# Kernel tuning notes

Measured on AMD Instinct MI355X. Metric: run time of the kernel, lower is better.

## Reference

```python
import jax, jax.numpy as jnp
import numpy as np

HID = 128
OUT = 5


def _gru_layer(x, kernel, rkernel, bias):
    # Keras GRU v2 semantics, reset_after=True, activation=tanh, recurrent_activation=sigmoid.
    # x: [B, T, F]; kernel: [F, 3H]; rkernel: [H, 3H]; bias: [2, 3H] (input bias, recurrent bias)
    b_in, b_rec = bias[0], bias[1]
    H = rkernel.shape[0]
    xw = jnp.einsum('btf,fh->bth', x, kernel) + b_in  # precompute input projections [B,T,3H]

    def step(h, xw_t):
        ri = h @ rkernel + b_rec                      # [B, 3H]
        xz, xr, xh = jnp.split(xw_t, 3, axis=-1)
        rz, rr, rh = jnp.split(ri, 3, axis=-1)
        z = jax.nn.sigmoid(xz + rz)
        r = jax.nn.sigmoid(xr + rr)
        hh = jnp.tanh(xh + r * rh)
        h_new = z * h + (1.0 - z) * hh
        return h_new, h_new

    h0 = jnp.zeros((x.shape[0], H), dtype=x.dtype)
    _, hs = jax.lax.scan(step, h0, jnp.swapaxes(xw, 0, 1))  # [T, B, H]
    return jnp.swapaxes(hs, 0, 1)                           # [B, T, H]


def setup_inputs() -> dict:
    key = jax.random.key(0)
    ks = jax.random.split(key, 12)
    B, T, F = 64, 2048, 128
    s = 1.0 / np.sqrt(F)
    inp = {"x": jax.random.normal(ks[0], (B, T, F), dtype=jnp.float32)}
    for i in range(3):
        fin = F if i == 0 else HID
        inp[f"k{i}"] = jax.random.normal(ks[1 + 3 * i], (fin, 3 * HID), dtype=jnp.float32) * s
        inp[f"rk{i}"] = jax.random.normal(ks[2 + 3 * i], (HID, 3 * HID), dtype=jnp.float32) * s
        inp[f"b{i}"] = jnp.zeros((2, 3 * HID), dtype=jnp.float32)
    inp["wo"] = jax.random.normal(ks[10], (HID, OUT), dtype=jnp.float32) * s
    inp["bo"] = jnp.zeros((OUT,), dtype=jnp.float32)
    return inp


def reference(x, k0, rk0, b0, k1, rk1, b1, k2, rk2, b2, wo, bo):
    h = _gru_layer(x, k0, rk0, b0)
    h = _gru_layer(h, k1, rk1, b1)
    h = _gru_layer(h, k2, rk2, b2)
    return h @ wo + bo  # [B, T, OUT]
```

## Files before the change

### kernel.cpp

```cpp
#include <hip/hip_runtime.h>
#include <hip/hip_bf16.h>
#include <hip/hip_fp16.h>


#define HID   128
#define H3    384
#define OUTD  5
#define CHK   16

typedef _Float16 f16x2 __attribute__((ext_vector_type(2)));
typedef _Float16 f16x8 __attribute__((ext_vector_type(8)));

__device__ __forceinline__ float fdot2(f16x2 a, f16x2 b, float c) {
#if __has_builtin(__builtin_amdgcn_fdot2)
    return __builtin_amdgcn_fdot2(a, b, c, false);
#else
    return fmaf((float)a.x, (float)b.x, fmaf((float)a.y, (float)b.y, c));
#endif
}

__device__ __forceinline__ float fexp2(float x) {
#if __has_builtin(__builtin_amdgcn_exp2f)
    return __builtin_amdgcn_exp2f(x);
#else
    return exp2f(x);
#endif
}

__device__ __forceinline__ float frcp(float x) {
#if __has_builtin(__builtin_amdgcn_rcpf)
    return __builtin_amdgcn_rcpf(x);
#else
    return 1.f / x;
#endif
}

__device__ __forceinline__ float fsigmoid(float x) {
    return frcp(1.f + fexp2(x * -1.4426950408889634f));
}

__device__ __forceinline__ float ftanh_(float x) {
    return fmaf(-2.f, frcp(1.f + fexp2(x * 2.8853900817779268f)), 1.f);
}

__device__ __forceinline__ void soft_barrier() {
    asm volatile("s_waitcnt lgkmcnt(0)\n\ts_barrier" ::: "memory");
}

__device__ __forceinline__ float quad_sum(float x) {
#if __has_builtin(__builtin_amdgcn_mov_dpp)
    int i1 = __builtin_amdgcn_mov_dpp(__float_as_int(x), 0xB1, 0xF, 0xF, true);
    x += __int_as_float(i1);
    int i2 = __builtin_amdgcn_mov_dpp(__float_as_int(x), 0x4E, 0xF, 0xF, true);
    x += __int_as_float(i2);
#else
    x += __shfl_xor(x, 1);
    x += __shfl_xor(x, 2);
#endif
    return x;
}

__global__ void zero_flags(int* f) {
    if (threadIdx.x < 192) f[threadIdx.x] = 0;
}

__global__ __launch_bounds__(512, 2) void gru_pipe(
    const float* __restrict__ x,
    const float* __restrict__ k0, const float* __restrict__ k1, const float* __restrict__ k2,
    const float* __restrict__ rk0, const float* __restrict__ rk1, const float* __restrict__ rk2,
    const float* __restrict__ b0, const float* __restrict__ b1, const float* __restrict__ b2,
    _Float16* __restrict__ hpl0, _Float16* __restrict__ hpl1, _Float16* __restrict__ hpl2,
    int* flags, int T)
{
    const int blk   = blockIdx.x;
    const int layer = blk >> 6;
    const int b     = blk & 63;
    const int t     = threadIdx.x;
    const int j     = t >> 2;
    const int kh    = t & 3;
    const int k0i   = kh * 32;
    const int NC    = T / CHK;

    const float* Kw = (layer == 0) ? k0  : (layer == 1) ? k1  : k2;
    const float* Rw = (layer == 0) ? rk0 : (layer == 1) ? rk1 : rk2;
    const float* Bs = (layer == 0) ? b0  : (layer == 1) ? b1  : b2;
    const _Float16* hin = (layer == 1) ? hpl0 : hpl1;
    _Float16* hout = (layer == 0) ? hpl0 : (layer == 1) ? hpl1 : hpl2;

    __shared__ __align__(16) _Float16 hb[2][HID];
    __shared__ __align__(16) _Float16 ins[2][CHK][HID];

    f16x2 wzR[16], wrR[16], whR[16], wzK[16], wrK[16], whK[16];
#pragma unroll
    for (int p = 0; p < 16; ++p) {
        const int k = k0i + 2 * p;
        const float* r0p = Rw + (size_t)k * H3;
        const float* r1p = Rw + (size_t)(k + 1) * H3;
        const float* k0p = Kw + (size_t)k * H3;
        const float* k1p = Kw + (size_t)(k + 1) * H3;
        f16x2 a;
        a.x = (_Float16)r0p[j];       a.y = (_Float16)r1p[j];       wzR[p] = a;
        a.x = (_Float16)r0p[j + 128]; a.y = (_Float16)r1p[j + 128]; wrR[p] = a;
        a.x = (_Float16)r0p[j + 256]; a.y = (_Float16)r1p[j + 256]; whR[p] = a;
        a.x = (_Float16)k0p[j];       a.y = (_Float16)k1p[j];       wzK[p] = a;
        a.x = (_Float16)k0p[j + 128]; a.y = (_Float16)k1p[j + 128]; wrK[p] = a;
        a.x = (_Float16)k0p[j + 256]; a.y = (_Float16)k1p[j + 256]; whK[p] = a;
    }
    const float bzK = Bs[j]       + Bs[384 + j];
    const float brK = Bs[128 + j] + Bs[384 + 128 + j];
    const float bhK = Bs[256 + j];
    const float bhR = Bs[384 + 256 + j];

    int* myflag = flags + layer * 64 + b;
    int* sflag  = flags + (layer - 1) * 64 + b;

    const float*    xb  = x    + (size_t)b * T * HID;
    const _Float16* hib = hin  + (size_t)b * T * HID;
    _Float16*       hob = hout + (size_t)b * T * HID;

    f16x2 sreg[2];
    auto stage_load = [&](int cc) {
#pragma unroll
        for (int i = 0; i < 2; ++i) {
            const int d  = t + 512 * i;
            const int rw = d >> 6;
            const int c2 = d & 63;
            const size_t off = (size_t)(cc * CHK + rw) * HID + 2 * c2;
            if (layer == 0) {
                const float2 v = *(const float2*)(xb + off);
                f16x2 o; o.x = (_Float16)v.x; o.y = (_Float16)v.y;
                sreg[i] = o;
            } else {
                sreg[i] = *(const f16x2*)(hib + off);
            }
        }
    };
    auto stage_write = [&](int cc) {
        const int slot = cc & 1;
#pragma unroll
        for (int i = 0; i < 2; ++i) {
            const int d  = t + 512 * i;
            const int rw = d >> 6;
            const int c2 = d & 63;
            *(f16x2*)(&ins[slot][rw][2 * c2]) = sreg[i];
        }
    };

    if (t < HID) { hb[0][t] = (_Float16)0.f; hb[1][t] = (_Float16)0.f; }

    if (layer > 0 && t == 0) {
        while (__hip_atomic_load(sflag, __ATOMIC_ACQUIRE, __HIP_MEMORY_SCOPE_AGENT) < CHK)
            __builtin_amdgcn_s_sleep(4);
    }
    __syncthreads();
    stage_load(0);
    stage_write(0);
    __syncthreads();

    float xz, xr, xh;
    {
        const f16x8* ip = (const f16x8*)(&ins[0][0][k0i]);
        float pz = 0.f, pr = 0.f, ph = 0.f;
#pragma unroll
        for (int i = 0; i < 4; ++i) {
            union { f16x8 v; f16x2 p[4]; } u;
            u.v = ip[i];
#pragma unroll
            for (int q = 0; q < 4; ++q) {
                pz = fdot2(u.p[q], wzK[4 * i + q], pz);
                pr = fdot2(u.p[q], wrK[4 * i + q], pr);
                ph = fdot2(u.p[q], whK[4 * i + q], ph);
            }
        }
        xz = quad_sum(pz) + bzK;
        xr = quad_sum(pr) + brK;
        xh = quad_sum(ph) + bhK;
    }

    float h_old = 0.f;

    for (int c = 0; c < NC; ++c) {
        __syncthreads();
        if (t == 0) {
            if (layer < 2 && c > 0)
                __hip_atomic_store(myflag, c * CHK, __ATOMIC_RELEASE, __HIP_MEMORY_SCOPE_AGENT);
            if (layer > 0 && c + 1 < NC) {
                while (__hip_atomic_load(sflag, __ATOMIC_ACQUIRE, __HIP_MEMORY_SCOPE_AGENT) < (c + 2) * CHK)
                    __builtin_amdgcn_s_sleep(4);
            }
        }
        __syncthreads();
        if (c + 1 < NC) stage_load(c + 1);

#pragma unroll 2
        for (int ts = 0; ts < CHK; ++ts) {
            const int tstep = c * CHK + ts;
            const int rbuf  = ts & 1;

            const f16x8* hp = (const f16x8*)(&hb[rbuf][k0i]);
            float sz = 0.f, sr = 0.f, sh = 0.f;
#pragma unroll
            for (int i = 0; i < 4; ++i) {
                union { f16x8 v; f16x2 p[4]; } u;
                u.v = hp[i];
#pragma unroll
                for (int q = 0; q < 4; ++q) {
                    sz = fdot2(u.p[q], wzR[4 * i + q], sz);
                    sr = fdot2(u.p[q], wrR[4 * i + q], sr);
                    sh = fdot2(u.p[q], whR[4 * i + q], sh);
                }
            }
            sz = quad_sum(sz); sr = quad_sum(sr); sh = quad_sum(sh);

            const float z  = fsigmoid(xz + sz);
            const float r  = fsigmoid(xr + sr);
            const float hh = ftanh_(xh + (sh + bhR) * r);
            const float hn = fmaf(z, h_old - hh, hh);
            h_old = hn;

            if (kh == 0) {
                hb[rbuf ^ 1][j] = (_Float16)hn;
                hob[(size_t)tstep * HID + j] = (_Float16)hn;
            }

            if (ts == 7 && c + 1 < NC) stage_write(c + 1);

            if (tstep + 1 < T) {
                const int tn = tstep + 1;
                const f16x8* ip = (const f16x8*)(&ins[(tn >> 4) & 1][tn & 15][k0i]);
                float pz = 0.f, pr = 0.f, ph = 0.f;
#pragma unroll
                for (int i = 0; i < 4; ++i) {
                    union { f16x8 v; f16x2 p[4]; } u;
                    u.v = ip[i];
#pragma unroll
                    for (int q = 0; q < 4; ++q) {
                        pz = fdot2(u.p[q], wzK[4 * i + q], pz);
                        pr = fdot2(u.p[q], wrK[4 * i + q], pr);
                        ph = fdot2(u.p[q], whK[4 * i + q], ph);
                    }
                }
                xz = quad_sum(pz) + bzK;
                xr = quad_sum(pr) + brK;
                xh = quad_sum(ph) + bhK;
            }

            soft_barrier();
        }
    }

    __syncthreads();
    if (t == 0 && layer < 2)
        __hip_atomic_store(myflag, T, __ATOMIC_RELEASE, __HIP_MEMORY_SCOPE_AGENT);
}

__global__ __launch_bounds__(256) void out_proj(
    const _Float16* __restrict__ Hf,
    const float* __restrict__ wo,
    const float* __restrict__ bo,
    float*       __restrict__ out,
    int R)
{
    const int r = blockIdx.x * 256 + threadIdx.x;
    if (r >= R) return;
    const f16x8* xp = (const f16x8*)(Hf + (size_t)r * HID);

    float a0 = bo[0], a1 = bo[1], a2 = bo[2], a3 = bo[3], a4 = bo[4];
#pragma unroll 4
    for (int c = 0; c < 16; ++c) {
        const f16x8 v = xp[c];
#pragma unroll
        for (int e = 0; e < 8; ++e) {
            const float xv = (float)v[e];
            const float* w = wo + (size_t)(8 * c + e) * OUTD;
            a0 = fmaf(xv, w[0], a0);
            a1 = fmaf(xv, w[1], a1);
            a2 = fmaf(xv, w[2], a2);
            a3 = fmaf(xv, w[3], a3);
            a4 = fmaf(xv, w[4], a4);
        }
    }
    float* op = out + (size_t)r * OUTD;
    op[0] = a0; op[1] = a1; op[2] = a2; op[3] = a3; op[4] = a4;
}

extern "C" void kernel_launch(void* const* d_in, const int* in_sizes, int n_in,
                              void* d_out, int out_size, void* d_ws, size_t ws_size,
                              hipStream_t stream) {
    const float* x   = (const float*)d_in[0];
    const float* k0  = (const float*)d_in[1];
    const float* rk0 = (const float*)d_in[2];
    const float* b0  = (const float*)d_in[3];
    const float* k1  = (const float*)d_in[4];
    const float* rk1 = (const float*)d_in[5];
    const float* b1  = (const float*)d_in[6];
    const float* k2  = (const float*)d_in[7];
    const float* rk2 = (const float*)d_in[8];
    const float* b2  = (const float*)d_in[9];
    const float* wo  = (const float*)d_in[10];
    const float* bo  = (const float*)d_in[11];
    float* out = (float*)d_out;

    const int BT = in_sizes[0] / HID;
    const int B  = 64;
    const int T  = BT / B;

    const size_t plane = (size_t)BT * HID * sizeof(_Float16);
    _Float16* hpl0 = (_Float16*)d_ws;
    _Float16* hpl1 = (_Float16*)((char*)d_ws + plane);
    _Float16* hpl2 = (_Float16*)((char*)d_ws + 2 * plane);
    int*      flags = (int*)((char*)d_ws + 3 * plane);

    zero_flags<<<1, 256, 0, stream>>>(flags);
    gru_pipe  <<<192, 512, 0, stream>>>(x, k0, k1, k2, rk0, rk1, rk2,
                                        b0, b1, b2, hpl0, hpl1, hpl2, flags, T);
    out_proj  <<<(BT + 255) / 256, 256, 0, stream>>>(hpl2, wo, bo, out, BT);
}
```

Before: 1.752 ms.

## Batch input projections per chunk into shared memory before the recurrent loop

Moves the per-timestep input projection (x·K) out of the serial recurrence. At the start of each 16-step chunk it computes the projections for all rows, two rows at a time for more ILP, and stores them in a new shared float buffer. The step loop then only reads three values from shared memory. This shortens the latency-critical per-step path, but adds 24KB of LDS, a barrier-separated batch phase per chunk, and quad_sum shuffles for six accumulators.

```diff
diff --git a/kernel.cpp b/kernel.cpp
--- a/kernel.cpp
+++ b/kernel.cpp
@@ -89,15 +89,16 @@
 
     __shared__ __align__(16) _Float16 hb[2][HID];
     __shared__ __align__(16) _Float16 ins[2][CHK][HID];
+    __shared__ __align__(16) float    xws[CHK][H3];
 
     f16x2 wzR[16], wrR[16], whR[16], wzK[16], wrK[16], whK[16];
 #pragma unroll
     for (int p = 0; p < 16; ++p) {
         const int k = k0i + 2 * p;
         const float* r0p = Rw + (size_t)k * H3;
-        const float* r1p = Rw + (size_t)(k + 1) * H3;
+        const float* r1p = r0p + H3;
         const float* k0p = Kw + (size_t)k * H3;
-        const float* k1p = Kw + (size_t)(k + 1) * H3;
+        const float* k1p = k0p + H3;
         f16x2 a;
         a.x = (_Float16)r0p[j];       a.y = (_Float16)r1p[j];       wzR[p] = a;
         a.x = (_Float16)r0p[j + 128]; a.y = (_Float16)r1p[j + 128]; wrR[p] = a;
@@ -106,10 +107,10 @@
         a.x = (_Float16)k0p[j + 128]; a.y = (_Float16)k1p[j + 128]; wrK[p] = a;
         a.x = (_Float16)k0p[j + 256]; a.y = (_Float16)k1p[j + 256]; whK[p] = a;
     }
-    const float bzK = Bs[j]       + Bs[384 + j];
-    const float brK = Bs[128 + j] + Bs[384 + 128 + j];
+    const float bzK = Bs[j]       + Bs[H3 + j];
+    const float brK = Bs[128 + j] + Bs[H3 + 128 + j];
     const float bhK = Bs[256 + j];
-    const float bhR = Bs[384 + 256 + j];
+    const float bhR = Bs[H3 + 256 + j];
 
     int* myflag = flags + layer * 64 + b;
     int* sflag  = flags + (layer - 1) * 64 + b;
@@ -155,27 +156,6 @@
     __syncthreads();
     stage_load(0);
     stage_write(0);
-    __syncthreads();
-
-    float xz, xr, xh;
-    {
-        const f16x8* ip = (const f16x8*)(&ins[0][0][k0i]);
-        float pz = 0.f, pr = 0.f, ph = 0.f;
-#pragma unroll
-        for (int i = 0; i < 4; ++i) {
-            union { f16x8 v; f16x2 p[4]; } u;
-            u.v = ip[i];
-#pragma unroll
-            for (int q = 0; q < 4; ++q) {
-                pz = fdot2(u.p[q], wzK[4 * i + q], pz);
-                pr = fdot2(u.p[q], wrK[4 * i + q], pr);
-                ph = fdot2(u.p[q], whK[4 * i + q], ph);
-            }
-        }
-        xz = quad_sum(pz) + bzK;
-        xr = quad_sum(pr) + brK;
-        xh = quad_sum(ph) + bhK;
-    }
 
     float h_old = 0.f;
 
@@ -192,10 +172,47 @@
         __syncthreads();
         if (c + 1 < NC) stage_load(c + 1);
 
+        {
+            const _Float16 (*insc)[HID] = ins[c & 1];
+#pragma unroll 2
+            for (int rp = 0; rp < 8; ++rp) {
+                const int r0 = 2 * rp, r1 = r0 + 1;
+                const f16x8* p0 = (const f16x8*)(&insc[r0][k0i]);
+                const f16x8* p1 = (const f16x8*)(&insc[r1][k0i]);
+                float az0 = 0.f, ar0 = 0.f, ah0 = 0.f;
+                float az1 = 0.f, ar1 = 0.f, ah1 = 0.f;
+#pragma unroll
+                for (int i = 0; i < 4; ++i) {
+                    union { f16x8 v; f16x2 p[4]; } u0, u1;
+                    u0.v = p0[i]; u1.v = p1[i];
+#pragma unroll
+                    for (int q = 0; q < 4; ++q) {
+                        az0 = fdot2(u0.p[q], wzK[4 * i + q], az0);
+                        az1 = fdot2(u1.p[q], wzK[4 * i + q], az1);
+                        ar0 = fdot2(u0.p[q], wrK[4 * i + q], ar0);
+                        ar1 = fdot2(u1.p[q], wrK[4 * i + q], ar1);
+                        ah0 = fdot2(u0.p[q], whK[4 * i + q], ah0);
+                        ah1 = fdot2(u1.p[q], whK[4 * i + q], ah1);
+                    }
+                }
+                az0 = quad_sum(az0); ar0 = quad_sum(ar0); ah0 = quad_sum(ah0);
+                az1 = quad_sum(az1); ar1 = quad_sum(ar1); ah1 = quad_sum(ah1);
+                if (kh == 0) {
+                    xws[r0][j] = az0 + bzK; xws[r0][128 + j] = ar0 + brK; xws[r0][256 + j] = ah0 + bhK;
+                    xws[r1][j] = az1 + bzK; xws[r1][128 + j] = ar1 + brK; xws[r1][256 + j] = ah1 + bhK;
+                }
+            }
+        }
+        soft_barrier();
+
 #pragma unroll 2
         for (int ts = 0; ts < CHK; ++ts) {
             const int tstep = c * CHK + ts;
             const int rbuf  = ts & 1;
+
+            const float xz = xws[ts][j];
+            const float xr = xws[ts][128 + j];
+            const float xh = xws[ts][256 + j];
 
             const f16x8* hp = (const f16x8*)(&hb[rbuf][k0i]);
             float sz = 0.f, sr = 0.f, sh = 0.f;
@@ -224,26 +241,6 @@
             }
 
             if (ts == 7 && c + 1 < NC) stage_write(c + 1);
-
-            if (tstep + 1 < T) {
-                const int tn = tstep + 1;
-                const f16x8* ip = (const f16x8*)(&ins[(tn >> 4) & 1][tn & 15][k0i]);
-                float pz = 0.f, pr = 0.f, ph = 0.f;
-#pragma unroll
-                for (int i = 0; i < 4; ++i) {
-                    union { f16x8 v; f16x2 p[4]; } u;
-                    u.v = ip[i];
-#pragma unroll
-                    for (int q = 0; q < 4; ++q) {
-                        pz = fdot2(u.p[q], wzK[4 * i + q], pz);
-                        pr = fdot2(u.p[q], wrK[4 * i + q], pr);
-                        ph = fdot2(u.p[q], whK[4 * i + q], ph);
-                    }
-                }
-                xz = quad_sum(pz) + bzK;
-                xr = quad_sum(pr) + brK;
-                xh = quad_sum(ph) + bhK;
-            }
 
             soft_barrier();
         }
```

Measured after the change: 1.910 ms. 1.09x slower.

## Batch 16 sequences per block and compute GRU gates with MFMA

Applied to the files above, without the earlier changes.

Replaces the per-sequence fdot2 GRU (192 blocks, one batch row each) with 12 blocks that each process 16 batch rows, running the recurrent and input projections as 16x16x32 f16 MFMA ops. Weights stay in registers as MFMA fragments, the hidden state sits in a swizzled shared buffer, and input rows are prefetched three steps ahead straight from global memory. A separate kernel converts x to fp16 up front. The aim is to cut the per-step latency of the serial recurrence by using matrix cores. In exchange only 12 CUs are occupied and each step is a chain of dependent MFMAs followed by a block barrier.

```diff
diff --git a/kernel.cpp b/kernel.cpp
--- a/kernel.cpp
+++ b/kernel.cpp
@@ -8,16 +8,10 @@
 #define OUTD  5
 #define CHK   16
 
-typedef _Float16 f16x2 __attribute__((ext_vector_type(2)));
 typedef _Float16 f16x8 __attribute__((ext_vector_type(8)));
-
-__device__ __forceinline__ float fdot2(f16x2 a, f16x2 b, float c) {
-#if __has_builtin(__builtin_amdgcn_fdot2)
-    return __builtin_amdgcn_fdot2(a, b, c, false);
-#else
-    return fmaf((float)a.x, (float)b.x, fmaf((float)a.y, (float)b.y, c));
-#endif
-}
+typedef float    f32x4 __attribute__((ext_vector_type(4)));
+
+#define SPLAT4(v) ((f32x4){(v), (v), (v), (v)})
 
 __device__ __forceinline__ float fexp2(float x) {
 #if __has_builtin(__builtin_amdgcn_exp2f)
@@ -47,25 +41,24 @@
     asm volatile("s_waitcnt lgkmcnt(0)\n\ts_barrier" ::: "memory");
 }
 
-__device__ __forceinline__ float quad_sum(float x) {
-#if __has_builtin(__builtin_amdgcn_mov_dpp)
-    int i1 = __builtin_amdgcn_mov_dpp(__float_as_int(x), 0xB1, 0xF, 0xF, true);
-    x += __int_as_float(i1);
-    int i2 = __builtin_amdgcn_mov_dpp(__float_as_int(x), 0x4E, 0xF, 0xF, true);
-    x += __int_as_float(i2);
-#else
-    x += __shfl_xor(x, 1);
-    x += __shfl_xor(x, 2);
-#endif
-    return x;
-}
-
 __global__ void zero_flags(int* f) {
-    if (threadIdx.x < 192) f[threadIdx.x] = 0;
-}
-
-__global__ __launch_bounds__(512, 2) void gru_pipe(
-    const float* __restrict__ x,
+    if (threadIdx.x < 12) f[threadIdx.x] = 0;
+}
+
+__global__ __launch_bounds__(256) void xcvt(
+    const float* __restrict__ x, _Float16* __restrict__ y, int n8) {
+    const int i = blockIdx.x * 256 + threadIdx.x;
+    if (i >= n8) return;
+    const float4 a = ((const float4*)x)[2 * i];
+    const float4 b = ((const float4*)x)[2 * i + 1];
+    f16x8 o;
+    o[0] = (_Float16)a.x; o[1] = (_Float16)a.y; o[2] = (_Float16)a.z; o[3] = (_Float16)a.w;
+    o[4] = (_Float16)b.x; o[5] = (_Float16)b.y; o[6] = (_Float16)b.z; o[7] = (_Float16)b.w;
+    ((f16x8*)y)[i] = o;
+}
+
+__global__ __launch_bounds__(512, 1) void gru12(
+    const _Float16* __restrict__ x16,
     const float* __restrict__ k0, const float* __restrict__ k1, const float* __restrict__ k2,
     const float* __restrict__ rk0, const float* __restrict__ rk1, const float* __restrict__ rk2,
     const float* __restrict__ b0, const float* __restrict__ b1, const float* __restrict__ b2,
@@ -73,111 +66,168 @@
     int* flags, int T)
 {
     const int blk   = blockIdx.x;
-    const int layer = blk >> 6;
-    const int b     = blk & 63;
+    const int layer = blk >> 2;
+    const int g     = blk & 3;
+    const int bg    = g * 16;
     const int t     = threadIdx.x;
-    const int j     = t >> 2;
-    const int kh    = t & 3;
-    const int k0i   = kh * 32;
+    const int w     = t >> 6;
+    const int l     = t & 63;
+    const int li    = l & 15;
+    const int lg    = l >> 4;
     const int NC    = T / CHK;
 
     const float* Kw = (layer == 0) ? k0  : (layer == 1) ? k1  : k2;
     const float* Rw = (layer == 0) ? rk0 : (layer == 1) ? rk1 : rk2;
     const float* Bs = (layer == 0) ? b0  : (layer == 1) ? b1  : b2;
-    const _Float16* hin = (layer == 1) ? hpl0 : hpl1;
+    const _Float16* xin = (layer == 0) ? x16 : (layer == 1) ? hpl0 : hpl1;
     _Float16* hout = (layer == 0) ? hpl0 : (layer == 1) ? hpl1 : hpl2;
 
-    __shared__ __align__(16) _Float16 hb[2][HID];
-    __shared__ __align__(16) _Float16 ins[2][CHK][HID];
-
-    f16x2 wzR[16], wrR[16], whR[16], wzK[16], wrK[16], whK[16];
-#pragma unroll
-    for (int p = 0; p < 16; ++p) {
-        const int k = k0i + 2 * p;
-        const float* r0p = Rw + (size_t)k * H3;
-        const float* r1p = Rw + (size_t)(k + 1) * H3;
-        const float* k0p = Kw + (size_t)k * H3;
-        const float* k1p = Kw + (size_t)(k + 1) * H3;
-        f16x2 a;
-        a.x = (_Float16)r0p[j];       a.y = (_Float16)r1p[j];       wzR[p] = a;
-        a.x = (_Float16)r0p[j + 128]; a.y = (_Float16)r1p[j + 128]; wrR[p] = a;
-        a.x = (_Float16)r0p[j + 256]; a.y = (_Float16)r1p[j + 256]; whR[p] = a;
-        a.x = (_Float16)k0p[j];       a.y = (_Float16)k1p[j];       wzK[p] = a;
-        a.x = (_Float16)k0p[j + 128]; a.y = (_Float16)k1p[j + 128]; wrK[p] = a;
-        a.x = (_Float16)k0p[j + 256]; a.y = (_Float16)k1p[j + 256]; whK[p] = a;
-    }
-    const float bzK = Bs[j]       + Bs[384 + j];
-    const float brK = Bs[128 + j] + Bs[384 + 128 + j];
-    const float bhK = Bs[256 + j];
-    const float bhR = Bs[384 + 256 + j];
-
-    int* myflag = flags + layer * 64 + b;
-    int* sflag  = flags + (layer - 1) * 64 + b;
-
-    const float*    xb  = x    + (size_t)b * T * HID;
-    const _Float16* hib = hin  + (size_t)b * T * HID;
-    _Float16*       hob = hout + (size_t)b * T * HID;
-
-    f16x2 sreg[2];
-    auto stage_load = [&](int cc) {
-#pragma unroll
-        for (int i = 0; i < 2; ++i) {
-            const int d  = t + 512 * i;
-            const int rw = d >> 6;
-            const int c2 = d & 63;
-            const size_t off = (size_t)(cc * CHK + rw) * HID + 2 * c2;
-            if (layer == 0) {
-                const float2 v = *(const float2*)(xb + off);
-                f16x2 o; o.x = (_Float16)v.x; o.y = (_Float16)v.y;
-                sreg[i] = o;
-            } else {
-                sreg[i] = *(const f16x2*)(hib + off);
+    __shared__ __align__(16) _Float16 Hs[2][2048];
+    _Float16* hsp = &Hs[0][0];
+
+    f16x8 RB[3][4], KB[3][4];
+#pragma unroll
+    for (int gi = 0; gi < 3; ++gi) {
+        const int col = 16 * w + 128 * gi + li;
+        const float* Rc = Rw + col;
+        const float* Kc = Kw + col;
+#pragma unroll
+        for (int kt = 0; kt < 4; ++kt) {
+            f16x8 rv, kv;
+#pragma unroll
+            for (int e = 0; e < 8; ++e) {
+                const int k = kt * 32 + lg * 8 + e;
+                rv[e] = (_Float16)Rc[(size_t)k * H3];
+                kv[e] = (_Float16)Kc[(size_t)k * H3];
             }
+            RB[gi][kt] = rv;
+            KB[gi][kt] = kv;
         }
-    };
-    auto stage_write = [&](int cc) {
-        const int slot = cc & 1;
-#pragma unroll
-        for (int i = 0; i < 2; ++i) {
-            const int d  = t + 512 * i;
-            const int rw = d >> 6;
-            const int c2 = d & 63;
-            *(f16x2*)(&ins[slot][rw][2 * c2]) = sreg[i];
-        }
-    };
-
-    if (t < HID) { hb[0][t] = (_Float16)0.f; hb[1][t] = (_Float16)0.f; }
+    }
+    const int uz = 16 * w + li;
+    const float bin0 = Bs[uz];
+    const float bin1 = Bs[128 + uz];
+    const float bin2 = Bs[256 + uz];
+    const float brc0 = Bs[H3 + uz];
+    const float brc1 = Bs[H3 + 128 + uz];
+    const float brc2 = Bs[H3 + 256 + uz];
+
+    int hr[4], hw[4];
+#pragma unroll
+    for (int kt = 0; kt < 4; ++kt) {
+        const int a = li * 256 + kt * 64 + lg * 16;
+        hr[kt] = a ^ ((li & 7) << 4);
+    }
+#pragma unroll
+    for (int q = 0; q < 4; ++q) {
+        const int b = lg * 4 + q;
+        const int a = b * 256 + uz * 2;
+        hw[q] = a ^ ((b & 7) << 4);
+    }
+
+    const _Float16* inb = xin + ((size_t)(bg + li) * T) * HID + lg * 8;
+
+    _Float16* hpq[4];
+#pragma unroll
+    for (int q = 0; q < 4; ++q)
+        hpq[q] = hout + ((size_t)(bg + lg * 4 + q) * T) * HID + uz;
+
+    int* myflag = flags + layer * 4 + g;
+    int* sflag  = flags + (layer - 1) * 4 + g;
+
+    ((float4*)hsp)[t] = float4{0.f, 0.f, 0.f, 0.f};
 
     if (layer > 0 && t == 0) {
         while (__hip_atomic_load(sflag, __ATOMIC_ACQUIRE, __HIP_MEMORY_SCOPE_AGENT) < CHK)
             __builtin_amdgcn_s_sleep(4);
     }
     __syncthreads();
-    stage_load(0);
-    stage_write(0);
-    __syncthreads();
-
-    float xz, xr, xh;
-    {
-        const f16x8* ip = (const f16x8*)(&ins[0][0][k0i]);
-        float pz = 0.f, pr = 0.f, ph = 0.f;
-#pragma unroll
-        for (int i = 0; i < 4; ++i) {
-            union { f16x8 v; f16x2 p[4]; } u;
-            u.v = ip[i];
-#pragma unroll
-            for (int q = 0; q < 4; ++q) {
-                pz = fdot2(u.p[q], wzK[4 * i + q], pz);
-                pr = fdot2(u.p[q], wrK[4 * i + q], pr);
-                ph = fdot2(u.p[q], whK[4 * i + q], ph);
-            }
-        }
-        xz = quad_sum(pz) + bzK;
-        xr = quad_sum(pr) + brK;
-        xh = quad_sum(ph) + bhK;
-    }
-
-    float h_old = 0.f;
+
+    f16x8 bb[2][4];
+    f32x4 XAz, XAr, XAh, XBz, XBr, XBh;
+    f32x4 hold = SPLAT4(0.f);
+
+#pragma unroll
+    for (int kt = 0; kt < 4; ++kt)
+        bb[0][kt] = *(const f16x8*)(inb + 0 * HID + kt * 32);
+    XAz = SPLAT4(bin0); XAr = SPLAT4(bin1); XAh = SPLAT4(bin2);
+    XAz = __builtin_amdgcn_mfma_f32_16x16x32_f16(bb[0][0], KB[0][0], XAz, 0, 0, 0);
+    XAz = __builtin_amdgcn_mfma_f32_16x16x32_f16(bb[0][1], KB[0][1], XAz, 0, 0, 0);
+    XAz = __builtin_amdgcn_mfma_f32_16x16x32_f16(bb[0][2], KB[0][2], XAz, 0, 0, 0);
+    XAz = __builtin_amdgcn_mfma_f32_16x16x32_f16(bb[0][3], KB[0][3], XAz, 0, 0, 0);
+    XAr = __builtin_amdgcn_mfma_f32_16x16x32_f16(bb[0][0], KB[1][0], XAr, 0, 0, 0);
+    XAr = __builtin_amdgcn_mfma_f32_16x16x32_f16(bb[0][1], KB[1][1], XAr, 0, 0, 0);
+    XAr = __builtin_amdgcn_mfma_f32_16x16x32_f16(bb[0][2], KB[1][2], XAr, 0, 0, 0);
+    XAr = __builtin_amdgcn_mfma_f32_16x16x32_f16(bb[0][3], KB[1][3], XAr, 0, 0, 0);
+    XAh = __builtin_amdgcn_mfma_f32_16x16x32_f16(bb[0][0], KB[2][0], XAh, 0, 0, 0);
+    XAh = __builtin_amdgcn_mfma_f32_16x16x32_f16(bb[0][1], KB[2][1], XAh, 0, 0, 0);
+    XAh = __builtin_amdgcn_mfma_f32_16x16x32_f16(bb[0][2], KB[2][2], XAh, 0, 0, 0);
+    XAh = __builtin_amdgcn_mfma_f32_16x16x32_f16(bb[0][3], KB[2][3], XAh, 0, 0, 0);
+#pragma unroll
+    for (int kt = 0; kt < 4; ++kt)
+        bb[1][kt] = *(const f16x8*)(inb + (size_t)1 * HID + kt * 32);
+#pragma unroll
+    for (int kt = 0; kt < 4; ++kt)
+        bb[0][kt] = *(const f16x8*)(inb + (size_t)2 * HID + kt * 32);
+
+#define GSTEP(P, XCz, XCr, XCh, XNz, XNr, XNh)                                  \
+    {                                                                           \
+        const int s_ = c * CHK + ts + (P);                                      \
+                                          \
+        const f16x8 ha0 = *(const f16x8*)(hsp + (P) * 2048 + (hr[0] >> 1));     \
+        const f16x8 ha1 = *(const f16x8*)(hsp + (P) * 2048 + (hr[1] >> 1));     \
+        const f16x8 ha2 = *(const f16x8*)(hsp + (P) * 2048 + (hr[2] >> 1));     \
+        const f16x8 ha3 = *(const f16x8*)(hsp + (P) * 2048 + (hr[3] >> 1));     \
+             \
+        XNz = SPLAT4(bin0); XNr = SPLAT4(bin1); XNh = SPLAT4(bin2);             \
+        XNz = __builtin_amdgcn_mfma_f32_16x16x32_f16(bb[1-(P)][0], KB[0][0], XNz, 0,0,0); \
+        XNz = __builtin_amdgcn_mfma_f32_16x16x32_f16(bb[1-(P)][1], KB[0][1], XNz, 0,0,0); \
+        XNz = __builtin_amdgcn_mfma_f32_16x16x32_f16(bb[1-(P)][2], KB[0][2], XNz, 0,0,0); \
+        XNz = __builtin_amdgcn_mfma_f32_16x16x32_f16(bb[1-(P)][3], KB[0][3], XNz, 0,0,0); \
+        XNr = __builtin_amdgcn_mfma_f32_16x16x32_f16(bb[1-(P)][0], KB[1][0], XNr, 0,0,0); \
+        XNr = __builtin_amdgcn_mfma_f32_16x16x32_f16(bb[1-(P)][1], KB[1][1], XNr, 0,0,0); \
+        XNr = __builtin_amdgcn_mfma_f32_16x16x32_f16(bb[1-(P)][2], KB[1][2], XNr, 0,0,0); \
+        XNr = __builtin_amdgcn_mfma_f32_16x16x32_f16(bb[1-(P)][3], KB[1][3], XNr, 0,0,0); \
+        XNh = __builtin_amdgcn_mfma_f32_16x16x32_f16(bb[1-(P)][0], KB[2][0], XNh, 0,0,0); \
+        XNh = __builtin_amdgcn_mfma_f32_16x16x32_f16(bb[1-(P)][1], KB[2][1], XNh, 0,0,0); \
+        XNh = __builtin_amdgcn_mfma_f32_16x16x32_f16(bb[1-(P)][2], KB[2][2], XNh, 0,0,0); \
+        XNh = __builtin_amdgcn_mfma_f32_16x16x32_f16(bb[1-(P)][3], KB[2][3], XNh, 0,0,0); \
+                              \
+        {   const int tl = (s_ + 3 < T) ? s_ + 3 : T - 1;                       \
+            const _Float16* ib_ = inb + (size_t)tl * HID;                       \
+            bb[1-(P)][0] = *(const f16x8*)(ib_);                                \
+            bb[1-(P)][1] = *(const f16x8*)(ib_ + 32);                           \
+            bb[1-(P)][2] = *(const f16x8*)(ib_ + 64);                           \
+            bb[1-(P)][3] = *(const f16x8*)(ib_ + 96);                           \
+        }                                                                       \
+                                               \
+        f32x4 Gz = SPLAT4(brc0), Gr = SPLAT4(brc1), Gh = SPLAT4(brc2);          \
+        Gz = __builtin_amdgcn_mfma_f32_16x16x32_f16(ha0, RB[0][0], Gz, 0,0,0);  \
+        Gz = __builtin_amdgcn_mfma_f32_16x16x32_f16(ha1, RB[0][1], Gz, 0,0,0);  \
+        Gz = __builtin_amdgcn_mfma_f32_16x16x32_f16(ha2, RB[0][2], Gz, 0,0,0);  \
+        Gz = __builtin_amdgcn_mfma_f32_16x16x32_f16(ha3, RB[0][3], Gz, 0,0,0);  \
+        Gr = __builtin_amdgcn_mfma_f32_16x16x32_f16(ha0, RB[1][0], Gr, 0,0,0);  \
+        Gr = __builtin_amdgcn_mfma_f32_16x16x32_f16(ha1, RB[1][1], Gr, 0,0,0);  \
+        Gr = __builtin_amdgcn_mfma_f32_16x16x32_f16(ha2, RB[1][2], Gr, 0,0,0);  \
+        Gr = __builtin_amdgcn_mfma_f32_16x16x32_f16(ha3, RB[1][3], Gr, 0,0,0);  \
+        Gh = __builtin_amdgcn_mfma_f32_16x16x32_f16(ha0, RB[2][0], Gh, 0,0,0);  \
+        Gh = __builtin_amdgcn_mfma_f32_16x16x32_f16(ha1, RB[2][1], Gh, 0,0,0);  \
+        Gh = __builtin_amdgcn_mfma_f32_16x16x32_f16(ha2, RB[2][2], Gh, 0,0,0);  \
+        Gh = __builtin_amdgcn_mfma_f32_16x16x32_f16(ha3, RB[2][3], Gh, 0,0,0);  \
+                                       \
+        _Pragma("unroll")                                                       \
+        for (int q = 0; q < 4; ++q) {                                           \
+            const float z_  = fsigmoid(Gz[q] + (XCz)[q]);                       \
+            const float r_  = fsigmoid(Gr[q] + (XCr)[q]);                       \
+            const float hh_ = ftanh_(fmaf(r_, Gh[q], (XCh)[q]));                \
+            const float hn_ = fmaf(z_, hold[q] - hh_, hh_);                     \
+            hold[q] = hn_;                                                      \
+            const _Float16 hf_ = (_Float16)hn_;                                 \
+            hsp[(1-(P)) * 2048 + (hw[q] >> 1)] = hf_;                           \
+            hpq[q][(size_t)s_ * HID] = hf_;                                     \
+        }                                                                       \
+        soft_barrier();                                                         \
+    }
 
     for (int c = 0; c < NC; ++c) {
         __syncthreads();
@@ -190,68 +240,17 @@
             }
         }
         __syncthreads();
-        if (c + 1 < NC) stage_load(c + 1);
-
-#pragma unroll 2
-        for (int ts = 0; ts < CHK; ++ts) {
-            const int tstep = c * CHK + ts;
-            const int rbuf  = ts & 1;
-
-            const f16x8* hp = (const f16x8*)(&hb[rbuf][k0i]);
-            float sz = 0.f, sr = 0.f, sh = 0.f;
-#pragma unroll
-            for (int i = 0; i < 4; ++i) {
-                union { f16x8 v; f16x2 p[4]; } u;
-                u.v = hp[i];
-#pragma unroll
-                for (int q = 0; q < 4; ++q) {
-                    sz = fdot2(u.p[q], wzR[4 * i + q], sz);
-                    sr = fdot2(u.p[q], wrR[4 * i + q], sr);
-                    sh = fdot2(u.p[q], whR[4 * i + q], sh);
-                }
-            }
-            sz = quad_sum(sz); sr = quad_sum(sr); sh = quad_sum(sh);
-
-            const float z  = fsigmoid(xz + sz);
-            const float r  = fsigmoid(xr + sr);
-            const float hh = ftanh_(xh + (sh + bhR) * r);
-            const float hn = fmaf(z, h_old - hh, hh);
-            h_old = hn;
-
-            if (kh == 0) {
-                hb[rbuf ^ 1][j] = (_Float16)hn;
-                hob[(size_t)tstep * HID + j] = (_Float16)hn;
-            }
-
-            if (ts == 7 && c + 1 < NC) stage_write(c + 1);
-
-            if (tstep + 1 < T) {
-                const int tn = tstep + 1;
-                const f16x8* ip = (const f16x8*)(&ins[(tn >> 4) & 1][tn & 15][k0i]);
-                float pz = 0.f, pr = 0.f, ph = 0.f;
-#pragma unroll
-                for (int i = 0; i < 4; ++i) {
-                    union { f16x8 v; f16x2 p[4]; } u;
-                    u.v = ip[i];
-#pragma unroll
-                    for (int q = 0; q < 4; ++q) {
-                        pz = fdot2(u.p[q], wzK[4 * i + q], pz);
-                        pr = fdot2(u.p[q], wrK[4 * i + q], pr);
-                        ph = fdot2(u.p[q], whK[4 * i + q], ph);
-                    }
-                }
-                xz = quad_sum(pz) + bzK;
-                xr = quad_sum(pr) + brK;
-                xh = quad_sum(ph) + bhK;
-            }
-
-            soft_barrier();
+
+        for (int ts = 0; ts < CHK; ts += 2) {
+            GSTEP(0, XAz, XAr, XAh, XBz, XBr, XBh)
+            GSTEP(1, XBz, XBr, XBh, XAz, XAr, XAh)
         }
     }
 
     __syncthreads();
     if (t == 0 && layer < 2)
         __hip_atomic_store(myflag, T, __ATOMIC_RELEASE, __HIP_MEMORY_SCOPE_AGENT);
+#undef GSTEP
 }
 
 __global__ __launch_bounds__(256) void out_proj(
@@ -272,12 +271,12 @@
 #pragma unroll
         for (int e = 0; e < 8; ++e) {
             const float xv = (float)v[e];
-            const float* w = wo + (size_t)(8 * c + e) * OUTD;
-            a0 = fmaf(xv, w[0], a0);
-            a1 = fmaf(xv, w[1], a1);
-            a2 = fmaf(xv, w[2], a2);
-            a3 = fmaf(xv, w[3], a3);
-            a4 = fmaf(xv, w[4], a4);
+            const float* wp = wo + (size_t)(8 * c + e) * OUTD;
+            a0 = fmaf(xv, wp[0], a0);
+            a1 = fmaf(xv, wp[1], a1);
+            a2 = fmaf(xv, wp[2], a2);
+            a3 = fmaf(xv, wp[3], a3);
+            a4 = fmaf(xv, wp[4], a4);
         }
     }
     float* op = out + (size_t)r * OUTD;
@@ -309,10 +308,14 @@
     _Float16* hpl0 = (_Float16*)d_ws;
     _Float16* hpl1 = (_Float16*)((char*)d_ws + plane);
     _Float16* hpl2 = (_Float16*)((char*)d_ws + 2 * plane);
-    int*      flags = (int*)((char*)d_ws + 3 * plane);
-
-    zero_flags<<<1, 256, 0, stream>>>(flags);
-    gru_pipe  <<<192, 512, 0, stream>>>(x, k0, k1, k2, rk0, rk1, rk2,
-                                        b0, b1, b2, hpl0, hpl1, hpl2, flags, T);
+    _Float16* x16  = (_Float16*)((char*)d_ws + 3 * plane);
+    int*      flags = (int*)((char*)d_ws + 4 * plane);
+
+    const int n8 = BT * HID / 8;
+
+    zero_flags<<<1, 64, 0, stream>>>(flags);
+    xcvt      <<<(n8 + 255) / 256, 256, 0, stream>>>(x, x16, n8);
+    gru12     <<<12, 512, 0, stream>>>(x16, k0, k1, k2, rk0, rk1, rk2,
+                                       b0, b1, b2, hpl0, hpl1, hpl2, flags, T);
     out_proj  <<<(BT + 255) / 256, 256, 0, stream>>>(hpl2, wo, bo, out, BT);
 }
```

Result: slower. 2.632 ms (+50.2%).
